# Performance work log

Hardware: AMD Instinct MI355X
Metric: run time of the kernel (lower is better)

The kernel has to match this reference:

```python
import jax, jax.numpy as jnp
import numpy as np

N_POL, N_TICK, N_COMM = 50000, 200000, 5000
N_STATES, N_SECTORS, N_INDUSTRIES = 50, 12, 150
EMB, HID, OUT = 32, 64, 32
N_NODES = N_POL + N_TICK + N_COMM
N_EDGES = 4_000_000


def setup_inputs() -> dict:
    key = jax.random.key(0)
    ks = jax.random.split(key, 24)
    s = lambda d: 1.0 / np.sqrt(d)
    inp = {
        "pol_features": jax.random.normal(ks[0], (N_POL, 7), jnp.float32),
        "state_ids": jax.random.randint(ks[1], (N_POL,), 0, N_STATES, jnp.int32),
        "sector_ids": jax.random.randint(ks[2], (N_TICK,), 0, N_SECTORS, jnp.int32),
        "industry_ids": jax.random.randint(ks[3], (N_TICK,), 0, N_INDUSTRIES, jnp.int32),
        "comp_extra": jax.random.normal(ks[4], (N_TICK, 1), jnp.float32),
        "edge_index": jax.random.randint(ks[5], (2, N_EDGES), 0, N_NODES, jnp.int32),
        "edge_weight": jax.random.uniform(ks[6], (N_EDGES,), jnp.float32),
        # learned params
        "pol_W": jax.random.normal(ks[7], (7, EMB), jnp.float32) * s(7),
        "pol_b": jnp.zeros((EMB,), jnp.float32),
        "state_emb": jax.random.normal(ks[8], (N_STATES, EMB), jnp.float32),
        "sector_emb": jax.random.normal(ks[9], (N_SECTORS, 8), jnp.float32),
        "industry_emb": jax.random.normal(ks[10], (N_INDUSTRIES, 8), jnp.float32),
        "comp_W": jax.random.normal(ks[11], (17, EMB), jnp.float32) * s(17),
        "comp_b": jnp.zeros((EMB,), jnp.float32),
        "comm_emb": jax.random.normal(ks[12], (N_COMM, EMB), jnp.float32),
        "ln_g": jnp.ones((EMB,), jnp.float32),
        "ln_b": jnp.zeros((EMB,), jnp.float32),
        "w1_rel": jax.random.normal(ks[13], (EMB, HID), jnp.float32) * s(EMB),
        "b1_rel": jnp.zeros((HID,), jnp.float32),
        "w1_root": jax.random.normal(ks[14], (EMB, HID), jnp.float32) * s(EMB),
        "w2_rel": jax.random.normal(ks[15], (HID, OUT), jnp.float32) * s(HID),
        "b2_rel": jnp.zeros((OUT,), jnp.float32),
        "w2_root": jax.random.normal(ks[16], (HID, OUT), jnp.float32) * s(HID),
    }
    return inp


def _layernorm(x, g, b, eps=1e-5):
    mu = jnp.mean(x, axis=-1, keepdims=True)
    var = jnp.mean(jnp.square(x - mu), axis=-1, keepdims=True)
    return (x - mu) * jax.lax.rsqrt(var + eps) * g + b


def _graph_conv(x, src, dst, ew, w_rel, b_rel, w_root):
    # PyG GraphConv: out = lin_rel(sum_{j->i} w_ji * x_j) + lin_root(x_i)
    msg = x[src] * ew[:, None]                                   # [E, d] gather
    agg = jax.ops.segment_sum(msg, dst, num_segments=x.shape[0])  # [N, d] scatter
    return agg @ w_rel + b_rel + x @ w_root


def reference(pol_features, state_ids, sector_ids, industry_ids, comp_extra,
              edge_index, edge_weight,
              pol_W, pol_b, state_emb, sector_emb, industry_emb, comp_W, comp_b,
              comm_emb, ln_g, ln_b, w1_rel, b1_rel, w1_root, w2_rel, b2_rel, w2_root):
    pol = jax.nn.relu(pol_features @ pol_W + pol_b) + state_emb[state_ids]
    comp_in = jnp.concatenate(
        [sector_emb[sector_ids], industry_emb[industry_ids], comp_extra], axis=1)  # [n_tick,17]
    comp = jax.nn.relu(comp_in @ comp_W + comp_b)
    x = jnp.concatenate([pol, comp, comm_emb], axis=0)  # [N, EMB]
    x = _layernorm(x, ln_g, ln_b)
    src, dst = edge_index[0], edge_index[1]
    x = jax.nn.relu(_graph_conv(x, src, dst, edge_weight, w1_rel, b1_rel, w1_root))
    # dropout omitted (eval mode)
    x = _graph_conv(x, src, dst, edge_weight, w2_rel, b2_rel, w2_root)
    return x
```

## Files before the change

kernel.cpp:

```cpp
#include <hip/hip_runtime.h>
#include <hip/hip_bf16.h>

#define N_POL  50000
#define N_TICK 200000
#define N_COMM 5000
#define N_NODES 255000
#define N_EDGES 4000000
#define EMB 32
#define HID 64
#define OUT_D 32

__global__ __launch_bounds__(256) void k_embed(
    const float* __restrict__ pol_features, const int* __restrict__ state_ids,
    const int* __restrict__ sector_ids, const int* __restrict__ industry_ids,
    const float* __restrict__ comp_extra,
    const float* __restrict__ pol_W, const float* __restrict__ pol_b,
    const float* __restrict__ state_emb, const float* __restrict__ sector_emb,
    const float* __restrict__ industry_emb, const float* __restrict__ comp_W,
    const float* __restrict__ comp_b, const float* __restrict__ comm_emb,
    const float* __restrict__ ln_g, const float* __restrict__ ln_b,
    float* __restrict__ x)
{
    int tid = blockIdx.x * 256 + threadIdx.x;
    int r = tid >> 5;
    int c = tid & 31;
    if (r >= N_NODES) return;

    float acc;
    if (r < N_POL) {
        acc = pol_b[c];
        #pragma unroll
        for (int k = 0; k < 7; ++k)
            acc = fmaf(pol_features[r*7 + k], pol_W[k*EMB + c], acc);
        acc = fmaxf(acc, 0.f);
        acc += state_emb[state_ids[r]*EMB + c];
    } else if (r < N_POL + N_TICK) {
        int i = r - N_POL;
        acc = comp_b[c];
        int sec = sector_ids[i], ind = industry_ids[i];
        #pragma unroll
        for (int k = 0; k < 8; ++k)
            acc = fmaf(sector_emb[sec*8 + k], comp_W[k*EMB + c], acc);
        #pragma unroll
        for (int k = 0; k < 8; ++k)
            acc = fmaf(industry_emb[ind*8 + k], comp_W[(8+k)*EMB + c], acc);
        acc = fmaf(comp_extra[i], comp_W[16*EMB + c], acc);
        acc = fmaxf(acc, 0.f);
    } else {
        acc = comm_emb[(r - N_POL - N_TICK)*EMB + c];
    }

    float s = acc;
    #pragma unroll
    for (int m = 16; m >= 1; m >>= 1) s += __shfl_xor(s, m, 32);
    float mu = s * (1.f/32.f);
    float d  = acc - mu;
    float v  = d * d;
    #pragma unroll
    for (int m = 16; m >= 1; m >>= 1) v += __shfl_xor(v, m, 32);
    v *= (1.f/32.f);
    x[r*EMB + c] = d * rsqrtf(v + 1e-5f) * ln_g[c] + ln_b[c];
}

__global__ __launch_bounds__(256) void k_hist(const int* __restrict__ ei,
                                              int* __restrict__ deg)
{
    int e = blockIdx.x * 256 + threadIdx.x;
    if (e >= N_EDGES) return;
    atomicAdd(&deg[ei[N_EDGES + e]], 1);
}

__global__ __launch_bounds__(256) void k_scan1(const int* __restrict__ deg,
                                               int* __restrict__ rowptr,
                                               int* __restrict__ bsum)
{
    __shared__ int s[256];
    int t = threadIdx.x;
    int base = blockIdx.x * 1024 + t * 4;
    int d0 = (base+0 < N_NODES) ? deg[base+0] : 0;
    int d1 = (base+1 < N_NODES) ? deg[base+1] : 0;
    int d2 = (base+2 < N_NODES) ? deg[base+2] : 0;
    int d3 = (base+3 < N_NODES) ? deg[base+3] : 0;
    int tsum = d0 + d1 + d2 + d3;
    s[t] = tsum;
    __syncthreads();
    for (int off = 1; off < 256; off <<= 1) {
        int v = (t >= off) ? s[t-off] : 0;
        __syncthreads();
        s[t] += v;
        __syncthreads();
    }
    int excl = s[t] - tsum;
    if (base+0 < N_NODES) rowptr[base+0] = excl;
    if (base+1 < N_NODES) rowptr[base+1] = excl + d0;
    if (base+2 < N_NODES) rowptr[base+2] = excl + d0 + d1;
    if (base+3 < N_NODES) rowptr[base+3] = excl + d0 + d1 + d2;
    if (t == 255) bsum[blockIdx.x] = s[255];
}

#define NBLK_SCAN 250

__global__ __launch_bounds__(256) void k_scan2(int* bsum)
{
    __shared__ int s[256];
    int t = threadIdx.x;
    int v = (t < NBLK_SCAN) ? bsum[t] : 0;
    s[t] = v;
    __syncthreads();
    for (int off = 1; off < 256; off <<= 1) {
        int u = (t >= off) ? s[t-off] : 0;
        __syncthreads();
        s[t] += u;
        __syncthreads();
    }
    if (t < NBLK_SCAN) bsum[t] = s[t] - v;
}

__global__ __launch_bounds__(256) void k_scan3(int* __restrict__ rowptr,
                                               const int* __restrict__ bsum)
{
    int i = blockIdx.x * 256 + threadIdx.x;
    if (i < N_NODES) rowptr[i] += bsum[i >> 10];
    if (i == 0) rowptr[N_NODES] = N_EDGES;
}

__global__ __launch_bounds__(256) void k_fill(const int* __restrict__ ei,
                                              const float* __restrict__ ew,
                                              const int* __restrict__ rowptr,
                                              int* __restrict__ cur,
                                              int2* __restrict__ ce)
{
    int e = blockIdx.x * 256 + threadIdx.x;
    if (e >= N_EDGES) return;
    int dst = ei[N_EDGES + e];
    int pos = rowptr[dst] + atomicAdd(&cur[dst], 1);
    ce[pos] = make_int2(ei[e], __float_as_int(ew[e]));
}

__global__ __launch_bounds__(256) void k_agg(const int* __restrict__ rowptr,
                                             const int2* __restrict__ ce,
                                             const float* __restrict__ feat,
                                             float* __restrict__ agg)
{
    int tid = blockIdx.x * 256 + threadIdx.x;
    int r = tid >> 5;
    int c = tid & 31;
    if (r >= N_NODES) return;
    int beg = rowptr[r], end = rowptr[r+1];
    float a0 = 0.f, a1 = 0.f, a2 = 0.f, a3 = 0.f;
    int i = beg;
    for (; i + 4 <= end; i += 4) {
        int2 e0 = ce[i], e1 = ce[i+1], e2 = ce[i+2], e3 = ce[i+3];
        a0 = fmaf(feat[(size_t)e0.x*EMB + c], __int_as_float(e0.y), a0);
        a1 = fmaf(feat[(size_t)e1.x*EMB + c], __int_as_float(e1.y), a1);
        a2 = fmaf(feat[(size_t)e2.x*EMB + c], __int_as_float(e2.y), a2);
        a3 = fmaf(feat[(size_t)e3.x*EMB + c], __int_as_float(e3.y), a3);
    }
    for (; i < end; ++i) {
        int2 e = ce[i];
        a0 = fmaf(feat[(size_t)e.x*EMB + c], __int_as_float(e.y), a0);
    }
    agg[(size_t)r*EMB + c] = (a0 + a1) + (a2 + a3);
}

__global__ __launch_bounds__(256) void k_conv1(
    const float* x, const float* __restrict__ agg,
    const float* __restrict__ w1_rel, const float* __restrict__ b1_rel,
    const float* __restrict__ w1_root, const float* __restrict__ w2_rel,
    float* __restrict__ x1, float* z)
{
    __shared__ float s_rel[32*64];
    __shared__ float s_root[32*64];
    __shared__ float s_w2[64*32];
    __shared__ float s_b1[64];
    for (int i = threadIdx.x; i < 2048; i += 256) {
        s_rel[i]  = w1_rel[i];
        s_root[i] = w1_root[i];
        s_w2[i]   = w2_rel[i];
    }
    if (threadIdx.x < 64) s_b1[threadIdx.x] = b1_rel[threadIdx.x];
    __syncthreads();

    int lane = threadIdx.x & 63;
    int wave = threadIdx.x >> 6;
    int c    = lane & 31;
    int half = lane >> 5;

    for (int r = blockIdx.x*4 + wave; r < N_NODES; r += gridDim.x*4) {
        float val = (lane < 32) ? x[r*EMB + lane] : agg[r*EMB + (lane - 32)];
        float acc = s_b1[lane];
        #pragma unroll
        for (int k = 0; k < 32; ++k) {
            float xk = __shfl(val, k, 64);
            float ak = __shfl(val, k + 32, 64);
            acc = fmaf(ak, s_rel[k*64 + lane], acc);
            acc = fmaf(xk, s_root[k*64 + lane], acc);
        }
        acc = fmaxf(acc, 0.f);
        x1[r*HID + lane] = acc;

        float part = 0.f;
        #pragma unroll
        for (int kk = 0; kk < 32; ++kk) {
            int k = half*32 + kk;
            part = fmaf(__shfl(acc, k, 64), s_w2[k*32 + c], part);
        }
        part += __shfl_xor(part, 32, 64);
        if (lane < 32) z[r*EMB + c] = part;
    }
}

__global__ __launch_bounds__(256) void k_conv2(
    const float* __restrict__ x1, const float* __restrict__ agg,
    const float* __restrict__ w2_root, const float* __restrict__ b2_rel,
    float* __restrict__ out)
{
    __shared__ float s_w[64*32];
    for (int i = threadIdx.x; i < 2048; i += 256) s_w[i] = w2_root[i];
    __syncthreads();

    int lane = threadIdx.x & 63;
    int wave = threadIdx.x >> 6;
    int c    = lane & 31;
    int half = lane >> 5;

    for (int r = blockIdx.x*4 + wave; r < N_NODES; r += gridDim.x*4) {
        float v = x1[r*HID + lane];
        float part = 0.f;
        #pragma unroll
        for (int kk = 0; kk < 32; ++kk) {
            int k = half*32 + kk;
            part = fmaf(__shfl(v, k, 64), s_w[k*32 + c], part);
        }
        part += __shfl_xor(part, 32, 64);
        if (lane < 32)
            out[r*OUT_D + c] = part + agg[r*EMB + c] + b2_rel[c];
    }
}

extern "C" void kernel_launch(void* const* d_in, const int* in_sizes, int n_in,
                              void* d_out, int out_size, void* d_ws, size_t ws_size,
                              hipStream_t stream) {
    const float* pol_features = (const float*)d_in[0];
    const int*   state_ids    = (const int*)  d_in[1];
    const int*   sector_ids   = (const int*)  d_in[2];
    const int*   industry_ids = (const int*)  d_in[3];
    const float* comp_extra   = (const float*)d_in[4];
    const int*   edge_index   = (const int*)  d_in[5];
    const float* edge_weight  = (const float*)d_in[6];
    const float* pol_W        = (const float*)d_in[7];
    const float* pol_b        = (const float*)d_in[8];
    const float* state_emb    = (const float*)d_in[9];
    const float* sector_emb   = (const float*)d_in[10];
    const float* industry_emb = (const float*)d_in[11];
    const float* comp_W       = (const float*)d_in[12];
    const float* comp_b       = (const float*)d_in[13];
    const float* comm_emb     = (const float*)d_in[14];
    const float* ln_g         = (const float*)d_in[15];
    const float* ln_b         = (const float*)d_in[16];
    const float* w1_rel       = (const float*)d_in[17];
    const float* b1_rel       = (const float*)d_in[18];
    const float* w1_root      = (const float*)d_in[19];
    const float* w2_rel       = (const float*)d_in[20];
    const float* b2_rel       = (const float*)d_in[21];
    const float* w2_root      = (const float*)d_in[22];

    float* x   = (float*)d_ws;
    float* x1  = x  + (size_t)N_NODES * EMB;
    float* agg = x1 + (size_t)N_NODES * HID;
    int2*  ce  = (int2*)(agg + (size_t)N_NODES * EMB);
    int*   rowptr = (int*)(ce + N_EDGES);
    int*   cur    = rowptr + N_NODES + 8;
    int*   bsum   = cur + N_NODES + 8;
    float* out = (float*)d_out;

    k_embed<<<(N_NODES*32 + 255)/256, 256, 0, stream>>>(
        pol_features, state_ids, sector_ids, industry_ids, comp_extra,
        pol_W, pol_b, state_emb, sector_emb, industry_emb, comp_W, comp_b,
        comm_emb, ln_g, ln_b, x);

    hipMemsetAsync(cur, 0, (size_t)N_NODES * sizeof(int), stream);
    k_hist<<<(N_EDGES + 255)/256, 256, 0, stream>>>(edge_index, cur);
    k_scan1<<<NBLK_SCAN, 256, 0, stream>>>(cur, rowptr, bsum);
    k_scan2<<<1, 256, 0, stream>>>(bsum);
    k_scan3<<<(N_NODES + 255)/256, 256, 0, stream>>>(rowptr, bsum);
    hipMemsetAsync(cur, 0, (size_t)N_NODES * sizeof(int), stream);
    k_fill<<<(N_EDGES + 255)/256, 256, 0, stream>>>(edge_index, edge_weight,
                                                    rowptr, cur, ce);

    k_agg<<<(N_NODES*32 + 255)/256, 256, 0, stream>>>(rowptr, ce, x, agg);
    k_conv1<<<4096, 256, 0, stream>>>(x, agg, w1_rel, b1_rel, w1_root, w2_rel,
                                      x1,  x);

    k_agg<<<(N_NODES*32 + 255)/256, 256, 0, stream>>>(rowptr, ce,  x, agg);
    k_conv2<<<4096, 256, 0, stream>>>(x1, agg, w2_root, b2_rel, out);
}
```

Baseline: 1.112 ms.

## Hold dense weights in registers and split conv1 from the w2_rel projection

The dense per-node matmuls now keep each lane's weight column in registers instead of LDS. Each wave reads its row's inputs as wave-uniform float4 loads, replacing the cross-lane shuffle broadcasts. The fused conv1 kernel is split into a conv1 kernel and a separate k_z kernel, so x1 is written and then read back from memory, plus one extra launch. The aim is to drop the shuffle and LDS-read overhead, at the cost of higher register pressure and extra global traffic.

```diff
diff --git a/kernel.cpp b/kernel.cpp
--- a/kernel.cpp
+++ b/kernel.cpp
@@ -164,77 +164,105 @@
 }
 
 __global__ __launch_bounds__(256) void k_conv1(
-    const float* x, const float* __restrict__ agg,
+    const float* __restrict__ x, const float* __restrict__ agg,
     const float* __restrict__ w1_rel, const float* __restrict__ b1_rel,
-    const float* __restrict__ w1_root, const float* __restrict__ w2_rel,
-    float* __restrict__ x1, float* z)
-{
-    __shared__ float s_rel[32*64];
-    __shared__ float s_root[32*64];
-    __shared__ float s_w2[64*32];
-    __shared__ float s_b1[64];
-    for (int i = threadIdx.x; i < 2048; i += 256) {
-        s_rel[i]  = w1_rel[i];
-        s_root[i] = w1_root[i];
-        s_w2[i]   = w2_rel[i];
-    }
-    if (threadIdx.x < 64) s_b1[threadIdx.x] = b1_rel[threadIdx.x];
-    __syncthreads();
-
+    const float* __restrict__ w1_root,
+    float* __restrict__ x1)
+{
     int lane = threadIdx.x & 63;
-    int wave = threadIdx.x >> 6;
+    int wid  = threadIdx.x >> 6;
+
+    float wr[32], wt[32];
+    #pragma unroll
+    for (int k = 0; k < 32; ++k) {
+        wr[k] = w1_rel[k*HID + lane];
+        wt[k] = w1_root[k*HID + lane];
+    }
+    float bias = b1_rel[lane];
+
+    int nw = gridDim.x * 4;
+    for (int r0 = blockIdx.x*4 + wid; r0 < N_NODES; r0 += nw) {
+        int r = __builtin_amdgcn_readfirstlane(r0);
+        const float4* xr = (const float4*)(x   + (size_t)r*EMB);
+        const float4* ar = (const float4*)(agg + (size_t)r*EMB);
+        float a0 = bias, a1 = 0.f, a2 = 0.f, a3 = 0.f;
+        #pragma unroll
+        for (int i = 0; i < 8; ++i) {
+            float4 xv = xr[i];
+            float4 av = ar[i];
+            a0 = fmaf(xv.x, wt[4*i+0], a0);  a0 = fmaf(av.x, wr[4*i+0], a0);
+            a1 = fmaf(xv.y, wt[4*i+1], a1);  a1 = fmaf(av.y, wr[4*i+1], a1);
+            a2 = fmaf(xv.z, wt[4*i+2], a2);  a2 = fmaf(av.z, wr[4*i+2], a2);
+            a3 = fmaf(xv.w, wt[4*i+3], a3);  a3 = fmaf(av.w, wr[4*i+3], a3);
+        }
+        x1[(size_t)r*HID + lane] = fmaxf((a0 + a1) + (a2 + a3), 0.f);
+    }
+}
+
+__global__ __launch_bounds__(256) void k_z(
+    const float* __restrict__ x1, const float* __restrict__ w2_rel,
+    float* __restrict__ z)
+{
+    int lane = threadIdx.x & 63;
+    int wid  = threadIdx.x >> 6;
     int c    = lane & 31;
     int half = lane >> 5;
 
-    for (int r = blockIdx.x*4 + wave; r < N_NODES; r += gridDim.x*4) {
-        float val = (lane < 32) ? x[r*EMB + lane] : agg[r*EMB + (lane - 32)];
-        float acc = s_b1[lane];
-        #pragma unroll
-        for (int k = 0; k < 32; ++k) {
-            float xk = __shfl(val, k, 64);
-            float ak = __shfl(val, k + 32, 64);
-            acc = fmaf(ak, s_rel[k*64 + lane], acc);
-            acc = fmaf(xk, s_root[k*64 + lane], acc);
+    float w[32];
+    #pragma unroll
+    for (int j = 0; j < 32; ++j) w[j] = w2_rel[(half*32 + j)*OUT_D + c];
+
+    int nw = gridDim.x * 4;
+    for (int r0 = blockIdx.x*4 + wid; r0 < N_NODES; r0 += nw) {
+        int r = __builtin_amdgcn_readfirstlane(r0);
+        const float4* xr = (const float4*)(x1 + (size_t)r*HID + half*32);
+        float p0 = 0.f, p1 = 0.f, p2 = 0.f, p3 = 0.f;
+        #pragma unroll
+        for (int i = 0; i < 8; ++i) {
+            float4 v = xr[i];
+            p0 = fmaf(v.x, w[4*i+0], p0);
+            p1 = fmaf(v.y, w[4*i+1], p1);
+            p2 = fmaf(v.z, w[4*i+2], p2);
+            p3 = fmaf(v.w, w[4*i+3], p3);
         }
-        acc = fmaxf(acc, 0.f);
-        x1[r*HID + lane] = acc;
-
-        float part = 0.f;
-        #pragma unroll
-        for (int kk = 0; kk < 32; ++kk) {
-            int k = half*32 + kk;
-            part = fmaf(__shfl(acc, k, 64), s_w2[k*32 + c], part);
-        }
+        float part = (p0 + p1) + (p2 + p3);
         part += __shfl_xor(part, 32, 64);
-        if (lane < 32) z[r*EMB + c] = part;
-    }
-}
-
-__global__ __launch_bounds__(256) void k_conv2(
+        if (lane < 32) z[(size_t)r*EMB + c] = part;
+    }
+}
+
+__global__ __launch_bounds__(256) void k_out(
     const float* __restrict__ x1, const float* __restrict__ agg,
     const float* __restrict__ w2_root, const float* __restrict__ b2_rel,
     float* __restrict__ out)
 {
-    __shared__ float s_w[64*32];
-    for (int i = threadIdx.x; i < 2048; i += 256) s_w[i] = w2_root[i];
-    __syncthreads();
-
     int lane = threadIdx.x & 63;
-    int wave = threadIdx.x >> 6;
+    int wid  = threadIdx.x >> 6;
     int c    = lane & 31;
     int half = lane >> 5;
 
-    for (int r = blockIdx.x*4 + wave; r < N_NODES; r += gridDim.x*4) {
-        float v = x1[r*HID + lane];
-        float part = 0.f;
-        #pragma unroll
-        for (int kk = 0; kk < 32; ++kk) {
-            int k = half*32 + kk;
-            part = fmaf(__shfl(v, k, 64), s_w[k*32 + c], part);
+    float w[32];
+    #pragma unroll
+    for (int j = 0; j < 32; ++j) w[j] = w2_root[(half*32 + j)*OUT_D + c];
+    float bias = b2_rel[c];
+
+    int nw = gridDim.x * 4;
+    for (int r0 = blockIdx.x*4 + wid; r0 < N_NODES; r0 += nw) {
+        int r = __builtin_amdgcn_readfirstlane(r0);
+        const float4* xr = (const float4*)(x1 + (size_t)r*HID + half*32);
+        float p0 = 0.f, p1 = 0.f, p2 = 0.f, p3 = 0.f;
+        #pragma unroll
+        for (int i = 0; i < 8; ++i) {
+            float4 v = xr[i];
+            p0 = fmaf(v.x, w[4*i+0], p0);
+            p1 = fmaf(v.y, w[4*i+1], p1);
+            p2 = fmaf(v.z, w[4*i+2], p2);
+            p3 = fmaf(v.w, w[4*i+3], p3);
         }
+        float part = (p0 + p1) + (p2 + p3);
         part += __shfl_xor(part, 32, 64);
         if (lane < 32)
-            out[r*OUT_D + c] = part + agg[r*EMB + c] + b2_rel[c];
+            out[(size_t)r*OUT_D + c] = part + agg[(size_t)r*EMB + c] + bias;
     }
 }
 
@@ -289,9 +317,9 @@
                                                     rowptr, cur, ce);
 
     k_agg<<<(N_NODES*32 + 255)/256, 256, 0, stream>>>(rowptr, ce, x, agg);
-    k_conv1<<<4096, 256, 0, stream>>>(x, agg, w1_rel, b1_rel, w1_root, w2_rel,
-                                      x1,  x);
+    k_conv1<<<4096, 256, 0, stream>>>(x, agg, w1_rel, b1_rel, w1_root, x1);
+    k_z<<<4096, 256, 0, stream>>>(x1, w2_rel,  x);
 
     k_agg<<<(N_NODES*32 + 255)/256, 256, 0, stream>>>(rowptr, ce,  x, agg);
-    k_conv2<<<4096, 256, 0, stream>>>(x1, agg, w2_root, b2_rel, out);
-}
+    k_out<<<4096, 256, 0, stream>>>(x1, agg, w2_root, b2_rel, out);
+}
```

Result: faster. 921.7 us (-17.1%).
